# Optimization experiments

Measured on AMD Instinct MI355X. Metric: run time of the kernel, lower is better.

## Reference

```python
import jax, jax.numpy as jnp
import numpy as np

N, FIN, H, FOUT = 4096, 128, 4, 64
NEG_INF = -1e9


def _xavier(key, shape):
    fan_in, fan_out = shape[-2], shape[-1]
    limit = float(np.sqrt(6.0 / (fan_in + fan_out)))
    return jax.random.uniform(key, shape, jnp.float32, -limit, limit)


def setup_inputs() -> dict:
    key = jax.random.key(0)
    ks = jax.random.split(key, 7)
    x = jax.random.normal(ks[0], (N, FIN), jnp.float32)
    u = jax.random.uniform(ks[1], (N, N))
    mask = jnp.where(u < 0.02, 0.0, NEG_INF).astype(jnp.float32)
    idx = jnp.arange(N)
    mask = mask.at[idx, idx].set(0.0)
    proj_param = _xavier(ks[2], (H, FIN, FOUT))          # per-head projection
    score_src = _xavier(ks[3], (H, FOUT, 1))             # scoring_fn_source (IMP1 layout)
    score_tgt = _xavier(ks[4], (H, FOUT, 1))             # scoring_fn_target
    skip_w = _xavier(ks[5], (H * FOUT, FIN))             # skip_proj Linear weight
    bias = jnp.zeros((H * FOUT,), jnp.float32)
    return {"x": x, "mask": mask, "proj_param": proj_param,
            "score_src": score_src, "score_tgt": score_tgt,
            "skip_w": skip_w, "bias": bias}


def reference(x, mask, proj_param, score_src, score_tgt, skip_w, bias):
    # project: [1,N,Fin] @ [H,Fin,Fout] -> [H,N,Fout]
    h = jnp.einsum('nf,hfo->hno', x, proj_param)
    # additive (Bahdanau-style) scores
    s_src = jnp.matmul(h, score_src)                     # [H,N,1]
    s_tgt = jnp.matmul(h, score_tgt)                     # [H,N,1]
    all_scores = jax.nn.leaky_relu(s_src + jnp.swapaxes(s_tgt, 1, 2), 0.2)  # [H,N,N]
    attn = jax.nn.softmax(all_scores + mask[None, :, :], axis=-1)           # [H,N,N]
    # aggregate: [H,N,N] @ [H,N,Fout] -> [N,H,Fout]
    out = jnp.einsum('hnm,hmo->nho', attn, h)
    # skip connection (dims differ: Fin != H*Fout -> use skip_proj)
    out = out + jnp.matmul(x, skip_w.T).reshape(N, H, FOUT)
    out = out.reshape(N, H * FOUT) + bias                # concat heads + bias
    return jax.nn.elu(out)
```

## Files before the change

kernel.cpp:

```cpp
#include <hip/hip_runtime.h>
#include <hip/hip_bf16.h>
#include <math.h>


#define NN   4096
#define FIN  128
#define NH   4
#define FO   64
#define HF   256
#define MAXNBR 384

__global__ __launch_bounds__(256) void k1_gemm(
        const float* __restrict__ x,
        const float* __restrict__ proj,
        const float* __restrict__ skw,
        const float* __restrict__ asrc,
        const float* __restrict__ atgt,
        float* __restrict__ h2, float* __restrict__ skip_ws,
        float* __restrict__ src4, float* __restrict__ tgt4) {
    __shared__ float sA[64 * 132];
    __shared__ float sB[128 * 64];
    const int tid = threadIdx.x;
    const int bc  = blockIdx.x;
    const int i0  = blockIdx.y * 64;

    {
        const float4* src = (const float4*)(x + (size_t)i0 * FIN);
        #pragma unroll
        for (int q = 0; q < 8; q++) {
            int s   = tid + q * 256;
            int row = s >> 5;
            int c4  = (s & 31) << 2;
            float4 v = src[s];
            float* d = sA + row * 132 + c4;
            d[0] = v.x; d[1] = v.y; d[2] = v.z; d[3] = v.w;
        }
    }
    if (bc < 4) {
        const float4* src = (const float4*)(proj + (size_t)bc * FIN * FO);
        #pragma unroll
        for (int q = 0; q < 8; q++) {
            int s = tid + q * 256;
            *(float4*)(sB + (size_t)s * 4) = src[s];
        }
    } else {
        const float* sw = skw + (size_t)(bc - 4) * 64 * FIN;
        #pragma unroll
        for (int q = 0; q < 8; q++) {
            int s  = tid + q * 256;
            int c  = s & 63;
            int k4 = (s >> 6) << 2;
            float4 v = *(const float4*)(sw + (size_t)c * FIN + k4);
            sB[(k4 + 0) * 64 + c] = v.x;
            sB[(k4 + 1) * 64 + c] = v.y;
            sB[(k4 + 2) * 64 + c] = v.z;
            sB[(k4 + 3) * 64 + c] = v.w;
        }
    }
    __syncthreads();

    const int tx = tid & 15, ty = tid >> 4;
    const int r0 = ty << 2, c0 = tx << 2;
    float acc[4][4] = {};
    #pragma unroll 2
    for (int k = 0; k < FIN; k += 4) {
        alignas(16) float a[4][4];
        alignas(16) float b[4][4];
        #pragma unroll
        for (int rr = 0; rr < 4; rr++)
            *(float4*)a[rr] = *(const float4*)(sA + (r0 + rr) * 132 + k);
        #pragma unroll
        for (int kk = 0; kk < 4; kk++)
            *(float4*)b[kk] = *(const float4*)(sB + (k + kk) * 64 + c0);
        #pragma unroll
        for (int kk = 0; kk < 4; kk++)
            #pragma unroll
            for (int rr = 0; rr < 4; rr++)
                #pragma unroll
                for (int cc = 0; cc < 4; cc++)
                    acc[rr][cc] = fmaf(a[rr][kk], b[kk][cc], acc[rr][cc]);
    }

    if (bc < 4) {
        float* dst = h2 + (size_t)i0 * HF + bc * 64;
        #pragma unroll
        for (int rr = 0; rr < 4; rr++)
            *(float4*)(dst + (size_t)(r0 + rr) * HF + c0) = *(float4*)acc[rr];

        float as[4], at[4];
        #pragma unroll
        for (int cc = 0; cc < 4; cc++) {
            as[cc] = asrc[bc * FO + c0 + cc];
            at[cc] = atgt[bc * FO + c0 + cc];
        }
        #pragma unroll
        for (int rr = 0; rr < 4; rr++) {
            float ps = acc[rr][0] * as[0] + acc[rr][1] * as[1]
                     + acc[rr][2] * as[2] + acc[rr][3] * as[3];
            float pt = acc[rr][0] * at[0] + acc[rr][1] * at[1]
                     + acc[rr][2] * at[2] + acc[rr][3] * at[3];
            #pragma unroll
            for (int off = 8; off >= 1; off >>= 1) {
                ps += __shfl_xor(ps, off, 64);
                pt += __shfl_xor(pt, off, 64);
            }
            if (tx == 0) {
                int i = i0 + r0 + rr;
                src4[(size_t)i * 4 + bc] = ps;
                tgt4[(size_t)i * 4 + bc] = pt;
            }
        }
    } else {
        float* dst = skip_ws + (size_t)i0 * HF + (bc - 4) * 64;
        #pragma unroll
        for (int rr = 0; rr < 4; rr++)
            *(float4*)(dst + (size_t)(r0 + rr) * HF + c0) = *(float4*)acc[rr];
    }
}

__global__ __launch_bounds__(256) void k2_attn(
        const unsigned int* __restrict__ mask,
        const float* __restrict__ h2,
        const float* __restrict__ skip_ws,
        const float* __restrict__ src4,
        const float* __restrict__ tgt4,
        const float* __restrict__ bias,
        float* __restrict__ out) {
    __shared__ int   s_nbr[MAXNBR];
    __shared__ float s_p[4][MAXNBR];
    __shared__ int   s_wt[4];
    __shared__ float s_red[4][4];
    __shared__ float s_m[4];
    __shared__ float s_l[4];
    const int tid  = threadIdx.x;
    const int lane = tid & 63, wid = tid >> 6;
    const int i    = blockIdx.x;

    const uint4* mrow = (const uint4*)(mask + (size_t)i * NN);
    uint4 mv0 = mrow[tid];
    uint4 mv1 = mrow[tid + 256];
    uint4 mv2 = mrow[tid + 512];
    uint4 mv3 = mrow[tid + 768];
    unsigned int hm = 0;
#define TESTW(w, b) hm |= (((w) & 0x7fffffffu) == 0u ? (1u << (b)) : 0u)
    TESTW(mv0.x, 0);  TESTW(mv0.y, 1);  TESTW(mv0.z, 2);  TESTW(mv0.w, 3);
    TESTW(mv1.x, 4);  TESTW(mv1.y, 5);  TESTW(mv1.z, 6);  TESTW(mv1.w, 7);
    TESTW(mv2.x, 8);  TESTW(mv2.y, 9);  TESTW(mv2.z, 10); TESTW(mv2.w, 11);
    TESTW(mv3.x, 12); TESTW(mv3.y, 13); TESTW(mv3.z, 14); TESTW(mv3.w, 15);
#undef TESTW
    int nh = __popc(hm);
    int v = nh;
    #pragma unroll
    for (int off = 1; off < 64; off <<= 1) {
        int t = __shfl_up(v, off, 64);
        if (lane >= off) v += t;
    }
    int excl = v - nh;
    if (lane == 63) s_wt[wid] = v;
    __syncthreads();
    const int t0 = s_wt[0], t1 = s_wt[1], t2 = s_wt[2], t3 = s_wt[3];
    const int cnt = min(t0 + t1 + t2 + t3, MAXNBR);
    int k = (wid > 0 ? t0 : 0) + (wid > 1 ? t1 : 0) + (wid > 2 ? t2 : 0) + excl;
    while (hm) {
        int b = __ffs(hm) - 1;
        hm &= hm - 1;
        int j = ((tid + ((b >> 2) << 8)) << 2) + (b & 3);
        if (k < MAXNBR) s_nbr[k] = j;
        k++;
    }
    __syncthreads();

    const float4 sv4 = *(const float4*)(src4 + (size_t)i * 4);
    const float sc0 = sv4.x, sc1 = sv4.y, sc2 = sv4.z, sc3 = sv4.w;
    float mx0 = -1e30f, mx1 = -1e30f, mx2 = -1e30f, mx3 = -1e30f;
    for (int kk = tid; kk < cnt; kk += 256) {
        int j = s_nbr[kk];
        float4 tg = *(const float4*)(tgt4 + (size_t)j * 4);
        float p0 = sc0 + tg.x; p0 = p0 > 0.f ? p0 : 0.2f * p0; s_p[0][kk] = p0; mx0 = fmaxf(mx0, p0);
        float p1 = sc1 + tg.y; p1 = p1 > 0.f ? p1 : 0.2f * p1; s_p[1][kk] = p1; mx1 = fmaxf(mx1, p1);
        float p2 = sc2 + tg.z; p2 = p2 > 0.f ? p2 : 0.2f * p2; s_p[2][kk] = p2; mx2 = fmaxf(mx2, p2);
        float p3 = sc3 + tg.w; p3 = p3 > 0.f ? p3 : 0.2f * p3; s_p[3][kk] = p3; mx3 = fmaxf(mx3, p3);
    }
    {
        float mxa[4] = {mx0, mx1, mx2, mx3};
        #pragma unroll
        for (int h = 0; h < 4; h++) {
            float m = mxa[h];
            #pragma unroll
            for (int off = 32; off >= 1; off >>= 1) m = fmaxf(m, __shfl_xor(m, off, 64));
            if (lane == 0) s_red[wid][h] = m;
        }
    }
    __syncthreads();
    if (tid < 4)
        s_m[tid] = fmaxf(fmaxf(s_red[0][tid], s_red[1][tid]),
                         fmaxf(s_red[2][tid], s_red[3][tid]));
    __syncthreads();

    const float m0 = s_m[0], m1 = s_m[1], m2 = s_m[2], m3 = s_m[3];
    float l0 = 0.f, l1 = 0.f, l2 = 0.f, l3 = 0.f;
    for (int kk = tid; kk < cnt; kk += 256) {
        float p0 = __expf(s_p[0][kk] - m0); s_p[0][kk] = p0; l0 += p0;
        float p1 = __expf(s_p[1][kk] - m1); s_p[1][kk] = p1; l1 += p1;
        float p2 = __expf(s_p[2][kk] - m2); s_p[2][kk] = p2; l2 += p2;
        float p3 = __expf(s_p[3][kk] - m3); s_p[3][kk] = p3; l3 += p3;
    }
    {
        float la[4] = {l0, l1, l2, l3};
        #pragma unroll
        for (int h = 0; h < 4; h++) {
            float l = la[h];
            #pragma unroll
            for (int off = 32; off >= 1; off >>= 1) l += __shfl_xor(l, off, 64);
            if (lane == 0) s_red[wid][h] = l;
        }
    }
    __syncthreads();
    if (tid < 4)
        s_l[tid] = s_red[0][tid] + s_red[1][tid] + s_red[2][tid] + s_red[3][tid];
    __syncthreads();

    const float* pp = s_p[wid];
    const float lv  = s_l[wid];
    const float inv = (cnt > 0 && lv > 0.f) ? 1.0f / lv : 0.0f;
    float acc = 0.f;
    int kk = 0;
    for (; kk + 8 <= cnt; kk += 8) {
        int   j0 = s_nbr[kk + 0], j1 = s_nbr[kk + 1], j2 = s_nbr[kk + 2], j3 = s_nbr[kk + 3];
        int   j4 = s_nbr[kk + 4], j5 = s_nbr[kk + 5], j6 = s_nbr[kk + 6], j7 = s_nbr[kk + 7];
        float p0 = pp[kk + 0], p1 = pp[kk + 1], p2 = pp[kk + 2], p3 = pp[kk + 3];
        float p4 = pp[kk + 4], p5 = pp[kk + 5], p6 = pp[kk + 6], p7 = pp[kk + 7];
        float h0 = h2[(size_t)j0 * HF + tid];
        float h1 = h2[(size_t)j1 * HF + tid];
        float h2v = h2[(size_t)j2 * HF + tid];
        float h3 = h2[(size_t)j3 * HF + tid];
        float h4 = h2[(size_t)j4 * HF + tid];
        float h5 = h2[(size_t)j5 * HF + tid];
        float h6 = h2[(size_t)j6 * HF + tid];
        float h7 = h2[(size_t)j7 * HF + tid];
        acc = fmaf(p0, h0, acc); acc = fmaf(p1, h1, acc);
        acc = fmaf(p2, h2v, acc); acc = fmaf(p3, h3, acc);
        acc = fmaf(p4, h4, acc); acc = fmaf(p5, h5, acc);
        acc = fmaf(p6, h6, acc); acc = fmaf(p7, h7, acc);
    }
    for (; kk < cnt; kk++)
        acc = fmaf(pp[kk], h2[(size_t)s_nbr[kk] * HF + tid], acc);

    float vv = acc * inv + skip_ws[(size_t)i * HF + tid] + bias[tid];
    vv = vv > 0.f ? vv : expm1f(vv);
    out[(size_t)i * HF + tid] = vv;
}

extern "C" void kernel_launch(void* const* d_in, const int* in_sizes, int n_in,
                              void* d_out, int out_size, void* d_ws, size_t ws_size,
                              hipStream_t stream) {
    const float*        x    = (const float*)d_in[0];
    const unsigned int* mask = (const unsigned int*)d_in[1];
    const float*        proj = (const float*)d_in[2];
    const float*        asrc = (const float*)d_in[3];
    const float*        atgt = (const float*)d_in[4];
    const float*        skw  = (const float*)d_in[5];
    const float*        bias = (const float*)d_in[6];
    float*              out  = (float*)d_out;

    float* ws      = (float*)d_ws;
    float* h2      = ws;
    float* skip_ws = ws + 1048576;
    float* src4    = ws + 2097152;
    float* tgt4    = ws + 2097152 + 16384;

    hipLaunchKernelGGL(k1_gemm, dim3(8, 64), dim3(256), 0, stream,
                       x, proj, skw, asrc, atgt, h2, skip_ws, src4, tgt4);
    hipLaunchKernelGGL(k2_attn, dim3(4096), dim3(256), 0, stream,
                       mask, h2, skip_ws, src4, tgt4, bias, out);
}
```

Before: 137.0 us.

## Store projected features as bf16 and make softmax per-wave with ballot compaction

The projected features h are now written in bf16, which halves the bytes of the gathered neighbour rows read during aggregation. Neighbour compaction now uses a wave ballot with mbcnt into a per-wave segment of 96 slots. Each wave does the softmax for its own head with shuffle reductions only, which removes several block-wide barriers and shared-memory reductions. The risks are bf16 rounding error in the aggregation and neighbours being dropped if any 1024-column segment holds more than 96 connections.

```diff
diff --git a/kernel.cpp b/kernel.cpp
--- a/kernel.cpp
+++ b/kernel.cpp
@@ -8,7 +8,17 @@
 #define NH   4
 #define FO   64
 #define HF   256
-#define MAXNBR 384
+#define SEG  96
+
+typedef unsigned short ushort_t;
+
+__device__ __forceinline__ ushort_t f2bf(float f) {
+    __hip_bfloat16 h = __float2bfloat16(f);
+    union { __hip_bfloat16 h; ushort_t u; } c; c.h = h; return c.u;
+}
+__device__ __forceinline__ float bf2f(ushort_t u) {
+    union { unsigned int i; float f; } c; c.i = ((unsigned int)u) << 16; return c.f;
+}
 
 __global__ __launch_bounds__(256) void k1_gemm(
         const float* __restrict__ x,
@@ -16,7 +26,7 @@
         const float* __restrict__ skw,
         const float* __restrict__ asrc,
         const float* __restrict__ atgt,
-        float* __restrict__ h2, float* __restrict__ skip_ws,
+        ushort_t* __restrict__ h2b, float* __restrict__ skip_ws,
         float* __restrict__ src4, float* __restrict__ tgt4) {
     __shared__ float sA[64 * 132];
     __shared__ float sB[128 * 64];
@@ -82,11 +92,13 @@
     }
 
     if (bc < 4) {
-        float* dst = h2 + (size_t)i0 * HF + bc * 64;
-        #pragma unroll
-        for (int rr = 0; rr < 4; rr++)
-            *(float4*)(dst + (size_t)(r0 + rr) * HF + c0) = *(float4*)acc[rr];
-
+        #pragma unroll
+        for (int rr = 0; rr < 4; rr++) {
+            ushort4 hv;
+            hv.x = f2bf(acc[rr][0]); hv.y = f2bf(acc[rr][1]);
+            hv.z = f2bf(acc[rr][2]); hv.w = f2bf(acc[rr][3]);
+            *(ushort4*)(h2b + (size_t)(i0 + r0 + rr) * HF + bc * 64 + c0) = hv;
+        }
         float as[4], at[4];
         #pragma unroll
         for (int cc = 0; cc < 4; cc++) {
@@ -120,135 +132,105 @@
 
 __global__ __launch_bounds__(256) void k2_attn(
         const unsigned int* __restrict__ mask,
-        const float* __restrict__ h2,
+        const ushort_t* __restrict__ h2b,
         const float* __restrict__ skip_ws,
         const float* __restrict__ src4,
         const float* __restrict__ tgt4,
         const float* __restrict__ bias,
         float* __restrict__ out) {
-    __shared__ int   s_nbr[MAXNBR];
-    __shared__ float s_p[4][MAXNBR];
-    __shared__ int   s_wt[4];
-    __shared__ float s_red[4][4];
-    __shared__ float s_m[4];
-    __shared__ float s_l[4];
+    __shared__ int   s_nbr[4 * SEG];
+    __shared__ float s_p[4][4 * SEG];
+    __shared__ int   s_ct[4];
     const int tid  = threadIdx.x;
-    const int lane = tid & 63, wid = tid >> 6;
+    const int lane = tid & 63, w = tid >> 6;
     const int i    = blockIdx.x;
 
     const uint4* mrow = (const uint4*)(mask + (size_t)i * NN);
-    uint4 mv0 = mrow[tid];
-    uint4 mv1 = mrow[tid + 256];
-    uint4 mv2 = mrow[tid + 512];
-    uint4 mv3 = mrow[tid + 768];
-    unsigned int hm = 0;
-#define TESTW(w, b) hm |= (((w) & 0x7fffffffu) == 0u ? (1u << (b)) : 0u)
-    TESTW(mv0.x, 0);  TESTW(mv0.y, 1);  TESTW(mv0.z, 2);  TESTW(mv0.w, 3);
-    TESTW(mv1.x, 4);  TESTW(mv1.y, 5);  TESTW(mv1.z, 6);  TESTW(mv1.w, 7);
-    TESTW(mv2.x, 8);  TESTW(mv2.y, 9);  TESTW(mv2.z, 10); TESTW(mv2.w, 11);
-    TESTW(mv3.x, 12); TESTW(mv3.y, 13); TESTW(mv3.z, 14); TESTW(mv3.w, 15);
-#undef TESTW
-    int nh = __popc(hm);
-    int v = nh;
-    #pragma unroll
-    for (int off = 1; off < 64; off <<= 1) {
-        int t = __shfl_up(v, off, 64);
-        if (lane >= off) v += t;
-    }
-    int excl = v - nh;
-    if (lane == 63) s_wt[wid] = v;
+    uint4 mv[4];
+    #pragma unroll
+    for (int s = 0; s < 4; s++) mv[s] = mrow[w * 256 + s * 64 + lane];
+
+    int base = 0;
+    #pragma unroll
+    for (int s = 0; s < 4; s++) {
+        unsigned int wv[4] = {mv[s].x, mv[s].y, mv[s].z, mv[s].w};
+        #pragma unroll
+        for (int e = 0; e < 4; e++) {
+            bool hit = (wv[e] & 0x7fffffffu) == 0u;
+            unsigned long long bal = __ballot(hit);
+            int pre = __builtin_amdgcn_mbcnt_hi(
+                          (unsigned int)(bal >> 32),
+                          __builtin_amdgcn_mbcnt_lo((unsigned int)bal, 0));
+            if (hit) {
+                int slot = base + pre;
+                if (slot < SEG)
+                    s_nbr[w * SEG + slot] = w * 1024 + s * 256 + lane * 4 + e;
+            }
+            base += (int)__popcll(bal);
+        }
+    }
+    if (lane == 0) s_ct[w] = base < SEG ? base : SEG;
     __syncthreads();
-    const int t0 = s_wt[0], t1 = s_wt[1], t2 = s_wt[2], t3 = s_wt[3];
-    const int cnt = min(t0 + t1 + t2 + t3, MAXNBR);
-    int k = (wid > 0 ? t0 : 0) + (wid > 1 ? t1 : 0) + (wid > 2 ? t2 : 0) + excl;
-    while (hm) {
-        int b = __ffs(hm) - 1;
-        hm &= hm - 1;
-        int j = ((tid + ((b >> 2) << 8)) << 2) + (b & 3);
-        if (k < MAXNBR) s_nbr[k] = j;
-        k++;
-    }
-    __syncthreads();
-
-    const float4 sv4 = *(const float4*)(src4 + (size_t)i * 4);
-    const float sc0 = sv4.x, sc1 = sv4.y, sc2 = sv4.z, sc3 = sv4.w;
-    float mx0 = -1e30f, mx1 = -1e30f, mx2 = -1e30f, mx3 = -1e30f;
-    for (int kk = tid; kk < cnt; kk += 256) {
-        int j = s_nbr[kk];
-        float4 tg = *(const float4*)(tgt4 + (size_t)j * 4);
-        float p0 = sc0 + tg.x; p0 = p0 > 0.f ? p0 : 0.2f * p0; s_p[0][kk] = p0; mx0 = fmaxf(mx0, p0);
-        float p1 = sc1 + tg.y; p1 = p1 > 0.f ? p1 : 0.2f * p1; s_p[1][kk] = p1; mx1 = fmaxf(mx1, p1);
-        float p2 = sc2 + tg.z; p2 = p2 > 0.f ? p2 : 0.2f * p2; s_p[2][kk] = p2; mx2 = fmaxf(mx2, p2);
-        float p3 = sc3 + tg.w; p3 = p3 > 0.f ? p3 : 0.2f * p3; s_p[3][kk] = p3; mx3 = fmaxf(mx3, p3);
-    }
-    {
-        float mxa[4] = {mx0, mx1, mx2, mx3};
-        #pragma unroll
-        for (int h = 0; h < 4; h++) {
-            float m = mxa[h];
-            #pragma unroll
-            for (int off = 32; off >= 1; off >>= 1) m = fmaxf(m, __shfl_xor(m, off, 64));
-            if (lane == 0) s_red[wid][h] = m;
-        }
-    }
-    __syncthreads();
-    if (tid < 4)
-        s_m[tid] = fmaxf(fmaxf(s_red[0][tid], s_red[1][tid]),
-                         fmaxf(s_red[2][tid], s_red[3][tid]));
-    __syncthreads();
-
-    const float m0 = s_m[0], m1 = s_m[1], m2 = s_m[2], m3 = s_m[3];
-    float l0 = 0.f, l1 = 0.f, l2 = 0.f, l3 = 0.f;
-    for (int kk = tid; kk < cnt; kk += 256) {
-        float p0 = __expf(s_p[0][kk] - m0); s_p[0][kk] = p0; l0 += p0;
-        float p1 = __expf(s_p[1][kk] - m1); s_p[1][kk] = p1; l1 += p1;
-        float p2 = __expf(s_p[2][kk] - m2); s_p[2][kk] = p2; l2 += p2;
-        float p3 = __expf(s_p[3][kk] - m3); s_p[3][kk] = p3; l3 += p3;
-    }
-    {
-        float la[4] = {l0, l1, l2, l3};
-        #pragma unroll
-        for (int h = 0; h < 4; h++) {
-            float l = la[h];
-            #pragma unroll
-            for (int off = 32; off >= 1; off >>= 1) l += __shfl_xor(l, off, 64);
-            if (lane == 0) s_red[wid][h] = l;
-        }
-    }
-    __syncthreads();
-    if (tid < 4)
-        s_l[tid] = s_red[0][tid] + s_red[1][tid] + s_red[2][tid] + s_red[3][tid];
-    __syncthreads();
-
-    const float* pp = s_p[wid];
-    const float lv  = s_l[wid];
-    const float inv = (cnt > 0 && lv > 0.f) ? 1.0f / lv : 0.0f;
+
+    const float sc = src4[(size_t)i * 4 + w];
+    float pmax = -1e30f;
+    int cts[4];
+    #pragma unroll
+    for (int s = 0; s < 4; s++) cts[s] = s_ct[s];
+    #pragma unroll
+    for (int s = 0; s < 4; s++) {
+        for (int kk = lane; kk < cts[s]; kk += 64) {
+            int j = s_nbr[s * SEG + kk];
+            float p = sc + tgt4[(size_t)j * 4 + w];
+            p = p > 0.f ? p : 0.2f * p;
+            s_p[w][s * SEG + kk] = p;
+            pmax = fmaxf(pmax, p);
+        }
+    }
+    #pragma unroll
+    for (int off = 32; off >= 1; off >>= 1)
+        pmax = fmaxf(pmax, __shfl_xor(pmax, off, 64));
+    float lsum = 0.f;
+    #pragma unroll
+    for (int s = 0; s < 4; s++) {
+        for (int kk = lane; kk < cts[s]; kk += 64) {
+            float e = __expf(s_p[w][s * SEG + kk] - pmax);
+            s_p[w][s * SEG + kk] = e;
+            lsum += e;
+        }
+    }
+    #pragma unroll
+    for (int off = 32; off >= 1; off >>= 1)
+        lsum += __shfl_xor(lsum, off, 64);
+    const float inv = lsum > 0.f ? 1.0f / lsum : 0.0f;
+
+    const int col = w * 64 + lane;
+    const ushort_t* hp = h2b + col;
+    const float* pp = s_p[w];
     float acc = 0.f;
-    int kk = 0;
-    for (; kk + 8 <= cnt; kk += 8) {
-        int   j0 = s_nbr[kk + 0], j1 = s_nbr[kk + 1], j2 = s_nbr[kk + 2], j3 = s_nbr[kk + 3];
-        int   j4 = s_nbr[kk + 4], j5 = s_nbr[kk + 5], j6 = s_nbr[kk + 6], j7 = s_nbr[kk + 7];
-        float p0 = pp[kk + 0], p1 = pp[kk + 1], p2 = pp[kk + 2], p3 = pp[kk + 3];
-        float p4 = pp[kk + 4], p5 = pp[kk + 5], p6 = pp[kk + 6], p7 = pp[kk + 7];
-        float h0 = h2[(size_t)j0 * HF + tid];
-        float h1 = h2[(size_t)j1 * HF + tid];
-        float h2v = h2[(size_t)j2 * HF + tid];
-        float h3 = h2[(size_t)j3 * HF + tid];
-        float h4 = h2[(size_t)j4 * HF + tid];
-        float h5 = h2[(size_t)j5 * HF + tid];
-        float h6 = h2[(size_t)j6 * HF + tid];
-        float h7 = h2[(size_t)j7 * HF + tid];
-        acc = fmaf(p0, h0, acc); acc = fmaf(p1, h1, acc);
-        acc = fmaf(p2, h2v, acc); acc = fmaf(p3, h3, acc);
-        acc = fmaf(p4, h4, acc); acc = fmaf(p5, h5, acc);
-        acc = fmaf(p6, h6, acc); acc = fmaf(p7, h7, acc);
-    }
-    for (; kk < cnt; kk++)
-        acc = fmaf(pp[kk], h2[(size_t)s_nbr[kk] * HF + tid], acc);
-
-    float vv = acc * inv + skip_ws[(size_t)i * HF + tid] + bias[tid];
+    #pragma unroll
+    for (int s = 0; s < 4; s++) {
+        const int ct = cts[s];
+        const int* nb = s_nbr + s * SEG;
+        const float* ps = pp + s * SEG;
+        int kk = 0;
+        for (; kk + 4 <= ct; kk += 4) {
+            int   j0 = nb[kk + 0], j1 = nb[kk + 1], j2 = nb[kk + 2], j3 = nb[kk + 3];
+            float p0 = ps[kk + 0], p1 = ps[kk + 1], p2 = ps[kk + 2], p3 = ps[kk + 3];
+            float h0 = bf2f(hp[(size_t)j0 * HF]);
+            float h1 = bf2f(hp[(size_t)j1 * HF]);
+            float h2v = bf2f(hp[(size_t)j2 * HF]);
+            float h3 = bf2f(hp[(size_t)j3 * HF]);
+            acc = fmaf(p0, h0, acc); acc = fmaf(p1, h1, acc);
+            acc = fmaf(p2, h2v, acc); acc = fmaf(p3, h3, acc);
+        }
+        for (; kk < ct; kk++)
+            acc = fmaf(ps[kk], bf2f(hp[(size_t)nb[kk] * HF]), acc);
+    }
+
+    float vv = acc * inv + skip_ws[(size_t)i * HF + col] + bias[col];
     vv = vv > 0.f ? vv : expm1f(vv);
-    out[(size_t)i * HF + tid] = vv;
+    out[(size_t)i * HF + col] = vv;
 }
 
 extern "C" void kernel_launch(void* const* d_in, const int* in_sizes, int n_in,
@@ -263,14 +245,14 @@
     const float*        bias = (const float*)d_in[6];
     float*              out  = (float*)d_out;
 
-    float* ws      = (float*)d_ws;
-    float* h2      = ws;
-    float* skip_ws = ws + 1048576;
-    float* src4    = ws + 2097152;
-    float* tgt4    = ws + 2097152 + 16384;
+    char* ws = (char*)d_ws;
+    ushort_t* h2b    = (ushort_t*)ws;
+    float*    skip_ws = (float*)(ws + (2u << 20));
+    float*    src4    = (float*)(ws + (6u << 20));
+    float*    tgt4    = (float*)(ws + (6u << 20) + (64u << 10));
 
     hipLaunchKernelGGL(k1_gemm, dim3(8, 64), dim3(256), 0, stream,
-                       x, proj, skw, asrc, atgt, h2, skip_ws, src4, tgt4);
+                       x, proj, skw, asrc, atgt, h2b, skip_ws, src4, tgt4);
     hipLaunchKernelGGL(k2_attn, dim3(4096), dim3(256), 0, stream,
-                       mask, h2, skip_ws, src4, tgt4, bias, out);
-}
+                       mask, h2b, skip_ws, src4, tgt4, bias, out);
+}
```

Measured after the change: 136.8 us. Within noise of the previous version (-0.2%).
